# Kernel optimization log

Measured on AMD Instinct MI355X. Metric: run time of the kernel, lower is better.

Reference implementation:

```python
import jax, jax.numpy as jnp
import numpy as np

N_HEADS = 16  # init kwarg n_heads
LN_EPS = 1e-5  # torch LayerNorm default eps


def setup_inputs() -> dict:
    key = jax.random.key(0)
    k1, k2, k3 = jax.random.split(key, 3)
    b, s, d = 4, 2048, 1024
    x0 = jax.random.normal(k1, (b, s, d), dtype=jnp.float32)
    # input_maps['x0']: Linear(d, 3*d, bias=False); stored as (in, out) so x @ W_in
    W_in = jax.random.normal(k2, (d, 3 * d), dtype=jnp.float32) * (d ** -0.5)
    # W_o: Linear(d, d, bias=False)
    W_o = jax.random.normal(k3, (d, d), dtype=jnp.float32) * (d ** -0.5)
    # key-padding mask: True = masked. All-valid (zeros) per spec.
    src_mask = jnp.zeros((b, s), dtype=bool)
    return {"x0": x0, "W_in": W_in, "W_o": W_o, "src_mask": src_mask}


def reference(x0, W_in, W_o, src_mask):
    b, s, d = x0.shape
    dh = d // N_HEADS  # per-head dim after chunking q,k,v
    x = jnp.einsum('bsd,de->bse', x0, W_in)  # (b, s, 3d)
    # rearrange 'b s (n_h 3*dh) -> b s n_h (3*dh)' then chunk into q,k,v
    x = x.reshape(b, s, N_HEADS, 3 * dh)
    q, k, v = jnp.split(x, 3, axis=-1)  # each (b, s, n_h, dh)
    logits = jnp.einsum('bqhd,bkhd->bhqk', q, k) * (dh ** -0.5)  # (b, n_h, s, s)
    causal = jnp.triu(jnp.ones((s, s), dtype=bool), k=1)
    mask = src_mask[:, None, None, :] | causal[None, None, :, :]
    logits = jnp.where(mask, -jnp.inf, logits)
    attn = jax.nn.softmax(logits, axis=-1)
    out = jnp.einsum('bhqk,bkhd->bqhd', attn, v).reshape(b, s, d)
    out = jnp.einsum('bsd,de->bse', out, W_o)
    y = out + x0  # residual with X[input_names[0]]
    # LayerNorm(out_dim, elementwise_affine=False)
    mu = jnp.mean(y, axis=-1, keepdims=True)
    var = jnp.var(y, axis=-1, keepdims=True)
    return (y - mu) * jax.lax.rsqrt(var + LN_EPS)
```

## Files before the change

kernel.cpp:

```cpp
#include <hip/hip_runtime.h>
#include <hip/hip_bf16.h>

typedef unsigned short u16;
typedef unsigned int u32;
typedef __attribute__((ext_vector_type(8))) short short8;
typedef __attribute__((ext_vector_type(4))) float f32x4;
typedef __attribute__((ext_vector_type(4))) int i32x4;

__device__ __forceinline__ float b2f(u16 u) {
    union { u32 i; float f; } x; x.i = ((u32)u) << 16; return x.f;
}
__device__ __forceinline__ u16 f2b(float f) {
    union { float f; u32 u; } x; x.f = f;
    u32 r = x.u + 0x7fffu + ((x.u >> 16) & 1u);
    return (u16)(r >> 16);
}
__device__ __forceinline__ u32 pkbf(float a, float b) {
    union { __hip_bfloat162 h; u32 u; } x;
    x.h = __float22bfloat162_rn(make_float2(a, b));
    return x.u;
}
__device__ __forceinline__ void async_cp16(const u16* g, u16* l) {
    __builtin_amdgcn_global_load_lds(
        (const __attribute__((address_space(1))) void*)g,
        (__attribute__((address_space(3))) void*)l, 16, 0, 0);
}

__global__ void probe_dtype(const u16* __restrict__ x, int* __restrict__ flag) {
    int bigf = 0;
    for (int i = threadIdx.x; i < 512; i += 64) {
        float v = fabsf(b2f(x[i]));
        if (!(v <= 1e6f)) bigf = 1;
    }
    int any = __any(bigf);
    if (threadIdx.x == 0) *flag = any ? 1 : 0;
}

__global__ __launch_bounds__(256) void canon(
    const void* __restrict__ src, u16* __restrict__ dst, int n,
    const int* __restrict__ flag)
{
    int i = (blockIdx.x * 256 + threadIdx.x) * 8;
    if (i >= n) return;
    if (*flag) {
        const float* s = (const float*)src + i;
        f32x4 a = *(const f32x4*)s;
        f32x4 b = *(const f32x4*)(s + 4);
        union { i32x4 v; u32 w[4]; } o;
        o.w[0] = pkbf(a[0], a[1]); o.w[1] = pkbf(a[2], a[3]);
        o.w[2] = pkbf(b[0], b[1]); o.w[3] = pkbf(b[2], b[3]);
        *(i32x4*)(dst + i) = o.v;
    } else {
        *(i32x4*)(dst + i) = *(const i32x4*)((const u16*)src + i);
    }
}

__global__ __launch_bounds__(256) void canon_t(
    const void* __restrict__ src, u16* __restrict__ dst, int Mdim, int Ndim,
    const int* __restrict__ flag)
{
    __shared__ __align__(16) u16 t[64 * 72];
    const int m0 = blockIdx.x * 64, n0 = blockIdx.y * 64;
    const int tid = threadIdx.x;
    const bool f = (*flag != 0);
#pragma unroll
    for (int p = 0; p < 2; ++p) {
        int s = tid + p * 256;
        int r = s >> 3, c0 = (s & 7) << 3;
        union { i32x4 v; u32 w[4]; } o;
        if (f) {
            const float* sp = (const float*)src + (size_t)(m0 + r) * Ndim + n0 + c0;
            f32x4 a = *(const f32x4*)sp, b = *(const f32x4*)(sp + 4);
            o.w[0] = pkbf(a[0], a[1]); o.w[1] = pkbf(a[2], a[3]);
            o.w[2] = pkbf(b[0], b[1]); o.w[3] = pkbf(b[2], b[3]);
        } else {
            o.v = *(const i32x4*)((const u16*)src + (size_t)(m0 + r) * Ndim + n0 + c0);
        }
        *(i32x4*)(t + r * 72 + c0) = o.v;
    }
    __syncthreads();
#pragma unroll
    for (int p = 0; p < 2; ++p) {
        int s = tid + p * 256;
        int oc = s >> 3, mc = (s & 7) << 3;
        union { i32x4 v; u16 h[8]; } o;
#pragma unroll
        for (int j = 0; j < 8; ++j) o.h[j] = t[(mc + j) * 72 + oc];
        *(i32x4*)(dst + (size_t)(n0 + oc) * Mdim + m0 + mc) = o.v;
    }
}

__global__ __launch_bounds__(256) void vtrans(
    const u16* __restrict__ qkv, u16* __restrict__ vT)
{
    __shared__ __align__(16) u16 t[64 * 72];
    const int bh = blockIdx.x, b = bh >> 4, h = bh & 15;
    const int s0 = blockIdx.y * 64;
    const int tid = threadIdx.x;
#pragma unroll
    for (int p = 0; p < 2; ++p) {
        int s = tid + p * 256;
        int r = s >> 3, c0 = (s & 7) << 3;
        *(i32x4*)(t + r * 72 + c0) =
            *(const i32x4*)(qkv + (size_t)(b * 2048 + s0 + r) * 3072 + h * 192 + 128 + c0);
    }
    __syncthreads();
#pragma unroll
    for (int p = 0; p < 2; ++p) {
        int s = tid + p * 256;
        int oc = s >> 3, mc = (s & 7) << 3;
        union { i32x4 v; u16 h[8]; } o;
#pragma unroll
        for (int j = 0; j < 8; ++j) o.h[j] = t[(mc + j) * 72 + oc];
        *(i32x4*)(vT + (size_t)(h * 64 + oc) * 8192 + b * 2048 + s0 + mc) = o.v;
    }
}

__global__ __launch_bounds__(256) void gemm_bf16(
    const u16* __restrict__ A, const u16* __restrict__ Bt, u16* __restrict__ C,
    int M, int N, int K)
{
    __shared__ __align__(16) u16 lA[128 * 64];
    __shared__ __align__(16) u16 lB[128 * 64];
    const int tid  = threadIdx.x;
    const int lane = tid & 63;
    const int wave = tid >> 6;
    const int la = lane & 15;
    const int qd = lane >> 4;
    const int m0 = blockIdx.x * 128, n0 = blockIdx.y * 128;
    const int wm = (wave & 1) * 64, wn = (wave >> 1) * 64;

    const int srow = lane >> 3;
    const int scol = ((lane & 7) ^ (lane >> 3)) << 3;
    const u16* gA = A  + (size_t)(m0 + wave * 32 + srow) * K + scol;
    const u16* gB = Bt + (size_t)(n0 + wave * 32 + srow) * K + scol;
    u16* lsA = lA + wave * 32 * 64;
    u16* lsB = lB + wave * 32 * 64;

    f32x4 acc[4][4];
    const f32x4 fz = {0.f, 0.f, 0.f, 0.f};
#pragma unroll
    for (int i = 0; i < 4; ++i)
#pragma unroll
        for (int j = 0; j < 4; ++j) acc[i][j] = fz;

    for (int k0 = 0; k0 < K; k0 += 64) {
        __syncthreads();
#pragma unroll
        for (int c = 0; c < 4; ++c) {
            async_cp16(gA + k0 + (size_t)(c * 8) * K, lsA + c * 8 * 64);
            async_cp16(gB + k0 + (size_t)(c * 8) * K, lsB + c * 8 * 64);
        }
        __syncthreads();

#pragma unroll
        for (int s = 0; s < 2; ++s) {
            short8 af[4], bf[4];
#pragma unroll
            for (int i = 0; i < 4; ++i) {
                int row = wm + i * 16 + la;
                af[i] = *(const short8*)(lA + row * 64 + (((s * 4 + qd) ^ (la & 7)) << 3));
            }
#pragma unroll
            for (int j = 0; j < 4; ++j) {
                int row = wn + j * 16 + la;
                bf[j] = *(const short8*)(lB + row * 64 + (((s * 4 + qd) ^ (la & 7)) << 3));
            }
#pragma unroll
            for (int i = 0; i < 4; ++i)
#pragma unroll
                for (int j = 0; j < 4; ++j)
                    acc[i][j] = __builtin_amdgcn_mfma_f32_16x16x32_bf16(
                        af[i], bf[j], acc[i][j], 0, 0, 0);
        }
    }

#pragma unroll
    for (int i = 0; i < 4; ++i)
#pragma unroll
        for (int j = 0; j < 4; ++j)
#pragma unroll
            for (int r = 0; r < 4; ++r) {
                int row = m0 + wm + i * 16 + qd * 4 + r;
                int col = n0 + wn + j * 16 + la;
                C[(size_t)row * N + col] = f2b(acc[i][j][r]);
            }
}

#define S_LEN 2048
#define D3 3072
#define NEG_BIG (-30000.0f)

__global__ __launch_bounds__(256, 5) void attn_fwd(
    const u16* __restrict__ qkv, const u16* __restrict__ vT,
    u16* __restrict__ outp)
{
    __shared__ __align__(16) u16 Ks[64 * 72];
    __shared__ __align__(16) u16 Vts[64 * 72];
    __shared__ __align__(16) u16 Ps[64 * 72];
    const int tid  = threadIdx.x;
    const int lane = tid & 63;
    const int wave = tid >> 6;
    const int la = lane & 15;
    const int qd = lane >> 4;
    const int lin = blockIdx.y * 16 + blockIdx.x;
    const int xcd = lin & 7, idx = lin >> 3;
    const int bh = xcd * 8 + (idx >> 4);
    const int px = idx & 15;
    const int b = bh >> 4, h = bh & 15;
    const size_t rowb = (size_t)b * S_LEN * D3;
    const int hq = h * 192;
    const u16* vTp = vT + (size_t)(h * 64) * 8192 + b * 2048;
    const f32x4 fz = {0.f, 0.f, 0.f, 0.f};

    const int srow0 = tid >> 3,         sseg0 = (tid & 7) << 3;
    const int srow1 = (tid + 256) >> 3, sseg1 = (tid & 7) << 3;

#pragma unroll
    for (int seg = 0; seg < 2; ++seg) {
        const int qt = seg == 0 ? px : 31 - px;
        const int q0 = qt * 64;
        const int qg = q0 + wave * 16 + la;

        short8 bq[2];
#pragma unroll
        for (int s = 0; s < 2; ++s) {
            union { short8 v; u16 h[8]; } u;
            u.v = *(const short8*)(qkv + rowb + (size_t)qg * D3 + hq + s * 32 + qd * 8);
#pragma unroll
            for (int j = 0; j < 8; ++j) u.h[j] = f2b(b2f(u.h[j]) * 0.125f);
            bq[s] = u.v;
        }

        f32x4 Oacc[4];
#pragma unroll
        for (int jd = 0; jd < 4; ++jd) Oacc[jd] = fz;
        float m_run = NEG_BIG, l_run = 0.f;

        i32x4 kreg[2], vreg[2];
        kreg[0] = *(const i32x4*)(qkv + rowb + (size_t)srow0 * D3 + hq + 64 + sseg0);
        kreg[1] = *(const i32x4*)(qkv + rowb + (size_t)srow1 * D3 + hq + 64 + sseg1);
        vreg[0] = *(const i32x4*)(vTp + (size_t)srow0 * 8192 + sseg0);
        vreg[1] = *(const i32x4*)(vTp + (size_t)srow1 * 8192 + sseg1);

        for (int kt = 0; kt <= qt; ++kt) {
            const int k0 = kt * 64;
            __syncthreads();
            *(i32x4*)(Ks  + srow0 * 72 + sseg0) = kreg[0];
            *(i32x4*)(Ks  + srow1 * 72 + sseg1) = kreg[1];
            *(i32x4*)(Vts + srow0 * 72 + sseg0) = vreg[0];
            *(i32x4*)(Vts + srow1 * 72 + sseg1) = vreg[1];
            if (kt < qt) {
                const int kn = k0 + 64;
                kreg[0] = *(const i32x4*)(qkv + rowb + (size_t)(kn + srow0) * D3 + hq + 64 + sseg0);
                kreg[1] = *(const i32x4*)(qkv + rowb + (size_t)(kn + srow1) * D3 + hq + 64 + sseg1);
                vreg[0] = *(const i32x4*)(vTp + (size_t)srow0 * 8192 + kn + sseg0);
                vreg[1] = *(const i32x4*)(vTp + (size_t)srow1 * 8192 + kn + sseg1);
            }
            __syncthreads();

            f32x4 sacc[4];
#pragma unroll
            for (int jm = 0; jm < 4; ++jm) sacc[jm] = fz;
#pragma unroll
            for (int s = 0; s < 2; ++s) {
#pragma unroll
                for (int jm = 0; jm < 4; ++jm) {
                    short8 ak = *(const short8*)(Ks + (jm * 16 + la) * 72 + s * 32 + qd * 8);
                    sacc[jm] = __builtin_amdgcn_mfma_f32_16x16x32_bf16(ak, bq[s], sacc[jm], 0, 0, 0);
                }
            }
            if (kt == qt) {
#pragma unroll
                for (int jm = 0; jm < 4; ++jm)
#pragma unroll
                    for (int r = 0; r < 4; ++r)
                        if (k0 + jm * 16 + qd * 4 + r > qg) sacc[jm][r] = NEG_BIG;
            }

            float mx = fmaxf(fmaxf(fmaxf(sacc[0][0], sacc[0][1]), fmaxf(sacc[0][2], sacc[0][3])),
                             fmaxf(fmaxf(sacc[1][0], sacc[1][1]), fmaxf(sacc[1][2], sacc[1][3])));
            mx = fmaxf(mx, fmaxf(fmaxf(fmaxf(sacc[2][0], sacc[2][1]), fmaxf(sacc[2][2], sacc[2][3])),
                                 fmaxf(fmaxf(sacc[3][0], sacc[3][1]), fmaxf(sacc[3][2], sacc[3][3]))));
            mx = fmaxf(mx, __shfl_xor(mx, 16));
            mx = fmaxf(mx, __shfl_xor(mx, 32));
            float mnew = fmaxf(m_run, mx);
            float al   = __expf(m_run - mnew);
            float ssum = 0.f;
#pragma unroll
            for (int jm = 0; jm < 4; ++jm)
#pragma unroll
                for (int r = 0; r < 4; ++r) {
                    float pv = __expf(sacc[jm][r] - mnew);
                    sacc[jm][r] = pv;
                    ssum += pv;
                }
            ssum += __shfl_xor(ssum, 16);
            ssum += __shfl_xor(ssum, 32);
            l_run = l_run * al + ssum;
            m_run = mnew;

#pragma unroll
            for (int jm = 0; jm < 4; ++jm) {
                uint2 w;
                w.x = pkbf(sacc[jm][0], sacc[jm][1]);
                w.y = pkbf(sacc[jm][2], sacc[jm][3]);
                *(uint2*)(Ps + (wave * 16 + la) * 72 + jm * 16 + qd * 4) = w;
            }

            float ar[4];
#pragma unroll
            for (int r = 0; r < 4; ++r) ar[r] = __shfl(al, qd * 4 + r);
#pragma unroll
            for (int jd = 0; jd < 4; ++jd)
#pragma unroll
                for (int r = 0; r < 4; ++r) Oacc[jd][r] *= ar[r];

#pragma unroll
            for (int s = 0; s < 2; ++s) {
                short8 ap = *(const short8*)(Ps + (wave * 16 + la) * 72 + s * 32 + qd * 8);
#pragma unroll
                for (int jd = 0; jd < 4; ++jd) {
                    short8 bv = *(const short8*)(Vts + (jd * 16 + la) * 72 + s * 32 + qd * 8);
                    Oacc[jd] = __builtin_amdgcn_mfma_f32_16x16x32_bf16(ap, bv, Oacc[jd], 0, 0, 0);
                }
            }
        }

#pragma unroll
        for (int r = 0; r < 4; ++r) {
            float lr = __shfl(l_run, qd * 4 + r);
            float inv = 1.f / lr;
            size_t orow = (size_t)(b * S_LEN + q0 + wave * 16 + qd * 4 + r) * 1024 + h * 64;
#pragma unroll
            for (int jd = 0; jd < 4; ++jd)
                outp[orow + jd * 16 + la] = f2b(Oacc[jd][r] * inv);
        }
    }
}

__global__ __launch_bounds__(256) void ln_residual(
    const u16* __restrict__ proj, const u16* __restrict__ x0,
    void* __restrict__ out, const int* __restrict__ flag)
{
    __shared__ float red[8];
    __shared__ float stats[2];
    const size_t base = (size_t)blockIdx.x * 1024 + threadIdx.x * 4;
    union { uint2 u; u16 s[4]; } pa, xa;
    pa.u = *(const uint2*)(proj + base);
    xa.u = *(const uint2*)(x0 + base);
    float y[4];
    float s1 = 0.f, s2 = 0.f;
#pragma unroll
    for (int j = 0; j < 4; ++j) {
        y[j] = b2f(pa.s[j]) + b2f(xa.s[j]);
        s1 += y[j];
        s2 += y[j] * y[j];
    }
#pragma unroll
    for (int off = 32; off > 0; off >>= 1) {
        s1 += __shfl_down(s1, off);
        s2 += __shfl_down(s2, off);
    }
    const int wave = threadIdx.x >> 6, lane = threadIdx.x & 63;
    if (lane == 0) { red[wave * 2] = s1; red[wave * 2 + 1] = s2; }
    __syncthreads();
    if (threadIdx.x == 0) {
        float S1 = red[0] + red[2] + red[4] + red[6];
        float S2 = red[1] + red[3] + red[5] + red[7];
        float mean = S1 * (1.f / 1024.f);
        float var  = fmaxf(S2 * (1.f / 1024.f) - mean * mean, 0.f);
        stats[0] = mean;
        stats[1] = rsqrtf(var + 1e-5f);
    }
    __syncthreads();
    float mean = stats[0], inv = stats[1];
    if (*flag) {
        f32x4 o;
#pragma unroll
        for (int j = 0; j < 4; ++j) o[j] = (y[j] - mean) * inv;
        *(f32x4*)((float*)out + base) = o;
    } else {
        union { uint2 u; u16 s[4]; } o;
#pragma unroll
        for (int j = 0; j < 4; ++j) o.s[j] = f2b((y[j] - mean) * inv);
        *(uint2*)((u16*)out + base) = o.u;
    }
}

extern "C" void kernel_launch(void* const* d_in, const int* in_sizes, int n_in,
                              void* d_out, int out_size, void* d_ws, size_t ws_size,
                              hipStream_t stream) {
    char* ws = (char*)d_ws;
    int* flag = (int*)ws;
    u16* cx0  = (u16*)(ws + 256);
    u16* wtin = cx0  + (size_t)8192 * 1024;
    u16* wto  = wtin + (size_t)3072 * 1024;
    u16* qkv  = wto  + (size_t)1024 * 1024;
    u16* vT   = qkv  + (size_t)8192 * 3072;
    u16* attn = vT   + (size_t)1024 * 8192;
    u16* proj = qkv;

    dim3 blk(256);
    probe_dtype<<<1, 64, 0, stream>>>((const u16*)d_in[0], flag);
    canon<<<4096, blk, 0, stream>>>(d_in[0], cx0, 8192 * 1024, flag);
    canon_t<<<dim3(16, 48), blk, 0, stream>>>(d_in[1], wtin, 1024, 3072, flag);
    canon_t<<<dim3(16, 16), blk, 0, stream>>>(d_in[2], wto,  1024, 1024, flag);
    gemm_bf16<<<dim3(64, 24), blk, 0, stream>>>(cx0, wtin, qkv, 8192, 3072, 1024);
    vtrans<<<dim3(64, 32), blk, 0, stream>>>(qkv, vT);
    attn_fwd<<<dim3(16, 64), blk, 0, stream>>>(qkv, vT, attn);
    gemm_bf16<<<dim3(64, 8), blk, 0, stream>>>(attn, wto, proj, 8192, 1024, 1024);
    ln_residual<<<dim3(8192), blk, 0, stream>>>(proj, cx0, d_out, flag);
}
```

Before: 299.3 us.

## Double-buffer K/V via async global-to-LDS copies with XOR swizzle and lazy rescale

```diff
diff --git a/kernel.cpp b/kernel.cpp
--- a/kernel.cpp
+++ b/kernel.cpp
@@ -191,13 +191,13 @@
 #define D3 3072
 #define NEG_BIG (-30000.0f)
 
-__global__ __launch_bounds__(256, 5) void attn_fwd(
+__global__ __launch_bounds__(256, 4) void attn_fwd(
     const u16* __restrict__ qkv, const u16* __restrict__ vT,
     u16* __restrict__ outp)
 {
-    __shared__ __align__(16) u16 Ks[64 * 72];
-    __shared__ __align__(16) u16 Vts[64 * 72];
-    __shared__ __align__(16) u16 Ps[64 * 72];
+    __shared__ __align__(16) u16 Ks[2 * 64 * 64];
+    __shared__ __align__(16) u16 Vts[2 * 64 * 64];
+    __shared__ __align__(16) u16 Ps[64 * 64];
     const int tid  = threadIdx.x;
     const int lane = tid & 63;
     const int wave = tid >> 6;
@@ -210,12 +210,17 @@
     const int b = bh >> 4, h = bh & 15;
     const size_t rowb = (size_t)b * S_LEN * D3;
     const int hq = h * 192;
-    const u16* vTp = vT + (size_t)(h * 64) * 8192 + b * 2048;
+    const u16* vTp = vT + (size_t)(h * 64) * 8192 + (size_t)b * 2048;
     const f32x4 fz = {0.f, 0.f, 0.f, 0.f};
 
-    const int srow0 = tid >> 3,         sseg0 = (tid & 7) << 3;
-    const int srow1 = (tid + 256) >> 3, sseg1 = (tid & 7) << 3;
-
+    const int srow = tid >> 3;
+    const int scol = ((tid & 7) ^ (srow & 7)) << 3;
+    const u16* gK = qkv + rowb + (size_t)srow * D3 + hq + 64 + scol;
+    const u16* gV = vTp + (size_t)srow * 8192 + scol;
+
+    const int swz = (la & 7);
+
+    int cur = 0;
 #pragma unroll
     for (int seg = 0; seg < 2; ++seg) {
         const int qt = seg == 0 ? px : 31 - px;
@@ -237,39 +242,43 @@
         for (int jd = 0; jd < 4; ++jd) Oacc[jd] = fz;
         float m_run = NEG_BIG, l_run = 0.f;
 
-        i32x4 kreg[2], vreg[2];
-        kreg[0] = *(const i32x4*)(qkv + rowb + (size_t)srow0 * D3 + hq + 64 + sseg0);
-        kreg[1] = *(const i32x4*)(qkv + rowb + (size_t)srow1 * D3 + hq + 64 + sseg1);
-        vreg[0] = *(const i32x4*)(vTp + (size_t)srow0 * 8192 + sseg0);
-        vreg[1] = *(const i32x4*)(vTp + (size_t)srow1 * 8192 + sseg1);
+        __syncthreads();
+#pragma unroll
+        for (int c = 0; c < 2; ++c) {
+            async_cp16(gK + (size_t)(c * 32) * D3, Ks + cur * 4096 + c * 2048 + wave * 512);
+            async_cp16(gV + (size_t)(c * 32) * 8192, Vts + cur * 4096 + c * 2048 + wave * 512);
+        }
 
         for (int kt = 0; kt <= qt; ++kt) {
             const int k0 = kt * 64;
             __syncthreads();
-            *(i32x4*)(Ks  + srow0 * 72 + sseg0) = kreg[0];
-            *(i32x4*)(Ks  + srow1 * 72 + sseg1) = kreg[1];
-            *(i32x4*)(Vts + srow0 * 72 + sseg0) = vreg[0];
-            *(i32x4*)(Vts + srow1 * 72 + sseg1) = vreg[1];
             if (kt < qt) {
                 const int kn = k0 + 64;
-                kreg[0] = *(const i32x4*)(qkv + rowb + (size_t)(kn + srow0) * D3 + hq + 64 + sseg0);
-                kreg[1] = *(const i32x4*)(qkv + rowb + (size_t)(kn + srow1) * D3 + hq + 64 + sseg1);
-                vreg[0] = *(const i32x4*)(vTp + (size_t)srow0 * 8192 + kn + sseg0);
-                vreg[1] = *(const i32x4*)(vTp + (size_t)srow1 * 8192 + kn + sseg1);
-            }
-            __syncthreads();
+#pragma unroll
+                for (int c = 0; c < 2; ++c) {
+                    async_cp16(gK + (size_t)(kn + c * 32) * D3,
+                               Ks + (cur ^ 1) * 4096 + c * 2048 + wave * 512);
+                    async_cp16(gV + (size_t)(c * 32) * 8192 + kn,
+                               Vts + (cur ^ 1) * 4096 + c * 2048 + wave * 512);
+                }
+            }
+            const u16* KsC  = Ks  + cur * 4096;
+            const u16* VtsC = Vts + cur * 4096;
 
             f32x4 sacc[4];
 #pragma unroll
             for (int jm = 0; jm < 4; ++jm) sacc[jm] = fz;
+            __builtin_amdgcn_s_setprio(1);
 #pragma unroll
             for (int s = 0; s < 2; ++s) {
 #pragma unroll
                 for (int jm = 0; jm < 4; ++jm) {
-                    short8 ak = *(const short8*)(Ks + (jm * 16 + la) * 72 + s * 32 + qd * 8);
+                    short8 ak = *(const short8*)(KsC + (jm * 16 + la) * 64 +
+                                                 (((s * 4 + qd) ^ swz) << 3));
                     sacc[jm] = __builtin_amdgcn_mfma_f32_16x16x32_bf16(ak, bq[s], sacc[jm], 0, 0, 0);
                 }
             }
+            __builtin_amdgcn_s_setprio(0);
             if (kt == qt) {
 #pragma unroll
                 for (int jm = 0; jm < 4; ++jm)
@@ -284,47 +293,57 @@
                                  fmaxf(fmaxf(sacc[3][0], sacc[3][1]), fmaxf(sacc[3][2], sacc[3][3]))));
             mx = fmaxf(mx, __shfl_xor(mx, 16));
             mx = fmaxf(mx, __shfl_xor(mx, 32));
-            float mnew = fmaxf(m_run, mx);
-            float al   = __expf(m_run - mnew);
+
+            const int skip = __all(mx <= m_run + 4.0f);
+            if (!skip) {
+                float mnew = fmaxf(m_run, mx);
+                float al   = __expf(m_run - mnew);
+                float ar[4];
+#pragma unroll
+                for (int r = 0; r < 4; ++r) ar[r] = __shfl(al, qd * 4 + r);
+#pragma unroll
+                for (int jd = 0; jd < 4; ++jd)
+#pragma unroll
+                    for (int r = 0; r < 4; ++r) Oacc[jd][r] *= ar[r];
+                l_run *= al;
+                m_run = mnew;
+            }
             float ssum = 0.f;
 #pragma unroll
             for (int jm = 0; jm < 4; ++jm)
 #pragma unroll
                 for (int r = 0; r < 4; ++r) {
-                    float pv = __expf(sacc[jm][r] - mnew);
+                    float pv = __expf(sacc[jm][r] - m_run);
                     sacc[jm][r] = pv;
                     ssum += pv;
                 }
             ssum += __shfl_xor(ssum, 16);
             ssum += __shfl_xor(ssum, 32);
-            l_run = l_run * al + ssum;
-            m_run = mnew;
+            l_run += ssum;
 
 #pragma unroll
             for (int jm = 0; jm < 4; ++jm) {
                 uint2 w;
                 w.x = pkbf(sacc[jm][0], sacc[jm][1]);
                 w.y = pkbf(sacc[jm][2], sacc[jm][3]);
-                *(uint2*)(Ps + (wave * 16 + la) * 72 + jm * 16 + qd * 4) = w;
-            }
-
-            float ar[4];
-#pragma unroll
-            for (int r = 0; r < 4; ++r) ar[r] = __shfl(al, qd * 4 + r);
-#pragma unroll
-            for (int jd = 0; jd < 4; ++jd)
-#pragma unroll
-                for (int r = 0; r < 4; ++r) Oacc[jd][r] *= ar[r];
-
+                *(uint2*)(Ps + (wave * 16 + la) * 64 +
+                          ((((jm * 2 + (qd >> 1)) ^ swz)) << 3) + ((qd & 1) << 2)) = w;
+            }
+
+            __builtin_amdgcn_s_setprio(1);
 #pragma unroll
             for (int s = 0; s < 2; ++s) {
-                short8 ap = *(const short8*)(Ps + (wave * 16 + la) * 72 + s * 32 + qd * 8);
+                short8 ap = *(const short8*)(Ps + (wave * 16 + la) * 64 +
+                                             (((s * 4 + qd) ^ swz) << 3));
 #pragma unroll
                 for (int jd = 0; jd < 4; ++jd) {
-                    short8 bv = *(const short8*)(Vts + (jd * 16 + la) * 72 + s * 32 + qd * 8);
+                    short8 bv = *(const short8*)(VtsC + (jd * 16 + la) * 64 +
+                                                 (((s * 4 + qd) ^ swz) << 3));
                     Oacc[jd] = __builtin_amdgcn_mfma_f32_16x16x32_bf16(ap, bv, Oacc[jd], 0, 0, 0);
                 }
             }
+            __builtin_amdgcn_s_setprio(0);
+            cur ^= 1;
         }
 
 #pragma unroll
```

Measured after the change: 283.2 us. 1.06x faster.
